# Kernel optimization log

Measured on AMD Instinct MI355X. Metric: run time of the kernel, lower is better.

## Reference

```python
import jax, jax.numpy as jnp
import numpy as np

V, H, NH, I, L, P = 32000, 1024, 16, 4096, 8, 2048
B, S = 2, 2048
DH = H // NH
EPS = 1e-5


def setup_inputs() -> dict:
    key = jax.random.key(0)
    ks = jax.random.split(key, 12)
    std = 0.02
    inp = {
        'input_ids': jax.random.randint(ks[0], (B, S), 0, V),
        'attention_mask': jnp.ones((B, S), dtype=jnp.float32),
        'tok_emb': jax.random.normal(ks[1], (V, H), jnp.float32) * std,
        'pos_emb': jax.random.normal(ks[2], (P, H), jnp.float32) * std,
        # per-layer params stacked on leading L dim (torch Linear convention: y = x @ W.T + b)
        'Wq': jax.random.normal(ks[3], (L, H, H), jnp.float32) * std,
        'bq': jnp.zeros((L, H), jnp.float32),
        'Wk': jax.random.normal(ks[4], (L, H, H), jnp.float32) * std,
        'bk': jnp.zeros((L, H), jnp.float32),
        'Wv': jax.random.normal(ks[5], (L, H, H), jnp.float32) * std,
        'bv': jnp.zeros((L, H), jnp.float32),
        'Wi': jax.random.normal(ks[6], (L, I, H), jnp.float32) * std,
        'bi': jnp.zeros((L, I), jnp.float32),
        'Wo': jax.random.normal(ks[7], (L, H, I), jnp.float32) * std,
        'bo': jnp.zeros((L, H), jnp.float32),
        'ln1_g': jnp.ones((L, H), jnp.float32),
        'ln1_b': jnp.zeros((L, H), jnp.float32),
        'ln2_g': jnp.ones((L, H), jnp.float32),
        'ln2_b': jnp.zeros((L, H), jnp.float32),
        'lnf_g': jnp.ones((H,), jnp.float32),
        'lnf_b': jnp.zeros((H,), jnp.float32),
        'Wlm': jax.random.normal(ks[8], (V, H), jnp.float32) * std,
    }
    return inp


def _layer_norm(x, g, b):
    m = jnp.mean(x, axis=-1, keepdims=True)
    v = jnp.var(x, axis=-1, keepdims=True)
    return (x - m) * jax.lax.rsqrt(v + EPS) * g + b


def reference(input_ids, attention_mask, tok_emb, pos_emb, Wq, bq, Wk, bk, Wv, bv,
              Wi, bi, Wo, bo, ln1_g, ln1_b, ln2_g, ln2_b, lnf_g, lnf_b, Wlm):
    b, s = input_ids.shape
    h = tok_emb[input_ids] + pos_emb[jnp.arange(s)][None, :, :]  # [B,S,H]
    mask = (1.0 - attention_mask)[:, None, None, :] * -10000.0   # [B,1,1,S]
    scale = 1.0 / (DH ** 0.5)

    def split_heads(x):  # [B,S,H] -> [B,NH,S,DH]
        return x.reshape(b, s, NH, DH).transpose(0, 2, 1, 3)

    def block(h, p):
        wq, bq_, wk, bk_, wv, bv_, wi, bi_, wo, bo_, g1, b1, g2, b2 = p
        q = split_heads(h @ wq.T + bq_)
        k = split_heads(h @ wk.T + bk_)
        v = split_heads(h @ wv.T + bv_)
        scores = jnp.einsum('bhqd,bhkd->bhqk', q, k) * scale + mask
        probs = jax.nn.softmax(scores, axis=-1)
        ctx = jnp.einsum('bhqk,bhkd->bhqd', probs, v)
        ctx = ctx.transpose(0, 2, 1, 3).reshape(b, s, H)
        h1 = _layer_norm(h + ctx, g1, b1)
        mlp = jax.nn.gelu(h1 @ wi.T + bi_, approximate=False) @ wo.T + bo_
        return _layer_norm(h1 + mlp, g2, b2), None

    h, _ = jax.lax.scan(block, h, (Wq, bq, Wk, bk, Wv, bv, Wi, bi, Wo, bo,
                                   ln1_g, ln1_b, ln2_g, ln2_b))
    h = _layer_norm(h, lnf_g, lnf_b)
    return h @ Wlm.T  # [B,S,V]
```

## Files before the change

kernel.cpp:

```cpp
#include <hip/hip_runtime.h>
#include <hip/hip_bf16.h>

#define V_ 32000
#define H_ 1024
#define NH_ 16
#define I_ 4096
#define L_ 8
#define B_ 2
#define S_ 2048
#define DH_ 64
#define M_ 4096
#define QS_ 3072

typedef __attribute__((ext_vector_type(4))) float f32x4;
typedef __attribute__((ext_vector_type(8))) short s16x8;

#define BARRIER() do { asm volatile("" ::: "memory"); __builtin_amdgcn_s_barrier(); asm volatile("" ::: "memory"); } while (0)
#define LGKM0()   do { asm volatile("s_waitcnt lgkmcnt(0)" ::: "memory"); __builtin_amdgcn_sched_barrier(0); } while (0)

__device__ __forceinline__ unsigned short f2b(float f) {
  union { float f; unsigned u; } x; x.f = f;
  return (unsigned short)((x.u + 0x7FFFu + ((x.u >> 16) & 1u)) >> 16);
}

__device__ __forceinline__ void gl_lds16(const unsigned short* g, unsigned short* l) {
  __builtin_amdgcn_global_load_lds(
      (__attribute__((address_space(1))) const void*)g,
      (__attribute__((address_space(3))) void*)l, 16, 0, 0);
}

__global__ __launch_bounds__(256) void wcvt(const float* __restrict__ src,
                                            unsigned short* __restrict__ dst) {
  size_t i = ((size_t)blockIdx.x * 256 + threadIdx.x) * 4;
  float4 v = *(const float4*)(src + i);
  ushort4 b;
  b.x = f2b(v.x); b.y = f2b(v.y); b.z = f2b(v.z); b.w = f2b(v.w);
  *(ushort4*)(dst + i) = b;
}

__global__ __launch_bounds__(256) void qkvcat_all(const float* __restrict__ q,
                                                  const float* __restrict__ k,
                                                  const float* __restrict__ v,
                                                  unsigned short* __restrict__ dst) {
  size_t i = ((size_t)blockIdx.x * 256 + threadIdx.x) * 4;
  size_t l = i / (3u * H_ * H_);
  size_t r = i - l * (3u * H_ * H_);
  const float* s; size_t off;
  if (r < (size_t)H_ * H_)          { s = q; off = l * H_ * H_ + r; }
  else if (r < 2u * H_ * H_)        { s = k; off = l * H_ * H_ + r - (size_t)H_ * H_; }
  else                              { s = v; off = l * H_ * H_ + r - 2u * H_ * H_; }
  float4 vv = *(const float4*)(s + off);
  ushort4 b;
  b.x = f2b(vv.x); b.y = f2b(vv.y); b.z = f2b(vv.z); b.w = f2b(vv.w);
  *(ushort4*)(dst + i) = b;
}

__global__ __launch_bounds__(256) void qkvcat(const float* __restrict__ q,
                                              const float* __restrict__ k,
                                              const float* __restrict__ v,
                                              unsigned short* __restrict__ dst) {
  int i = (blockIdx.x * 256 + threadIdx.x) * 4;
  const float* s; int off;
  if (i < H_ * H_)          { s = q; off = i; }
  else if (i < 2 * H_ * H_) { s = k; off = i - H_ * H_; }
  else                      { s = v; off = i - 2 * H_ * H_; }
  float4 vv = *(const float4*)(s + off);
  ushort4 b;
  b.x = f2b(vv.x); b.y = f2b(vv.y); b.z = f2b(vv.z); b.w = f2b(vv.w);
  *(ushort4*)(dst + i) = b;
}

__global__ __launch_bounds__(256) void bcat(const float* __restrict__ bq,
                                            const float* __restrict__ bk,
                                            const float* __restrict__ bv,
                                            float* __restrict__ dst) {
  int i = blockIdx.x * 256 + threadIdx.x;
  int l = i / (3 * H_), r = i - l * 3 * H_;
  int p = r >> 10, c = r & (H_ - 1);
  const float* s = (p == 0) ? bq : ((p == 1) ? bk : bv);
  dst[i] = s[l * H_ + c];
}

__global__ __launch_bounds__(256) void embed_kernel(
    const int* __restrict__ ids, const float* __restrict__ tok,
    const float* __restrict__ pos, float* __restrict__ h,
    unsigned short* __restrict__ xbf)
{
  int row = blockIdx.x;
  int c4 = threadIdx.x;
  int id = ids[row];
  int s = row & (S_ - 1);
  float4 tv = ((const float4*)(tok + (size_t)id * H_))[c4];
  float4 pv = ((const float4*)(pos + (size_t)s * H_))[c4];
  float4 v; v.x = tv.x + pv.x; v.y = tv.y + pv.y; v.z = tv.z + pv.z; v.w = tv.w + pv.w;
  ((float4*)(h + (size_t)row * H_))[c4] = v;
  ushort4 b; b.x = f2b(v.x); b.y = f2b(v.y); b.z = f2b(v.z); b.w = f2b(v.w);
  ((ushort4*)(xbf + (size_t)row * H_))[c4] = b;
}

template<int EPI>
__global__ __launch_bounds__(256) void gemm_bt(
    const unsigned short* __restrict__ A, const unsigned short* __restrict__ Wb,
    const float* __restrict__ bias, float* __restrict__ outf,
    unsigned short* __restrict__ outb, int M, int N, int K)
{
  __shared__ unsigned short As[128][32];
  __shared__ unsigned short Bs[128][32];
  int t = threadIdx.x;
  int lane = t & 63, wid = t >> 6;
  int m0 = blockIdx.x * 128, n0 = blockIdx.y * 128;
  int wm = (wid >> 1) * 64, wn = (wid & 1) * 64;
  int fr = lane & 15, kh = (lane >> 4) * 8;
  int lrow = lane >> 2, lcol = (lane & 3) * 8;

  f32x4 acc[4][4] = {};

  const unsigned short* Abase = A  + (size_t)(m0 + wid * 32 + lrow) * K + lcol;
  const unsigned short* Bbase = Wb + (size_t)(n0 + wid * 32 + lrow) * K + lcol;
  unsigned short* AL0 = &As[wid * 32][0];
  unsigned short* AL1 = &As[wid * 32 + 16][0];
  unsigned short* BL0 = &Bs[wid * 32][0];
  unsigned short* BL1 = &Bs[wid * 32 + 16][0];

  for (int k0 = 0; k0 < K; k0 += 32) {
    gl_lds16(Abase + k0,                     AL0);
    gl_lds16(Abase + k0 + (size_t)16 * K,    AL1);
    gl_lds16(Bbase + k0,                     BL0);
    gl_lds16(Bbase + k0 + (size_t)16 * K,    BL1);
    __syncthreads();
    s16x8 af[4], bfr[4];
    #pragma unroll
    for (int i = 0; i < 4; ++i) af[i]  = *(const s16x8*)(&As[wm + i * 16 + fr][kh]);
    #pragma unroll
    for (int j = 0; j < 4; ++j) bfr[j] = *(const s16x8*)(&Bs[wn + j * 16 + fr][kh]);
    #pragma unroll
    for (int i = 0; i < 4; ++i)
      #pragma unroll
      for (int j = 0; j < 4; ++j)
        acc[i][j] = __builtin_amdgcn_mfma_f32_16x16x32_bf16(af[i], bfr[j], acc[i][j], 0, 0, 0);
    __syncthreads();
  }

  int fq = lane >> 4;
  #pragma unroll
  for (int i = 0; i < 4; ++i) {
    #pragma unroll
    for (int j = 0; j < 4; ++j) {
      #pragma unroll
      for (int r = 0; r < 4; ++r) {
        int row = m0 + wm + i * 16 + fq * 4 + r;
        int col = n0 + wn + j * 16 + fr;
        float v = acc[i][j][r] + (bias ? bias[col] : 0.f);
        if (EPI == 0) {
          outf[(size_t)row * N + col] = v;
        } else if (EPI == 1) {
          float ge = 0.5f * v * (1.0f + erff(v * 0.70710678118f));
          outb[(size_t)row * N + col] = f2b(ge);
        } else {
          outb[(size_t)row * N + col] = f2b(v);
        }
      }
    }
  }
}

template<int EPI>
__global__ __launch_bounds__(512, 2) void gemm256(
    const unsigned short* __restrict__ A, const unsigned short* __restrict__ Wb,
    const float* __restrict__ bias, float* __restrict__ outf,
    unsigned short* __restrict__ outb, int M, int N, int K)
{
  __shared__ unsigned short ASm[2][16384];
  __shared__ unsigned short BSm[2][16384];

  const int t = threadIdx.x;
  const int lane = t & 63, wid = t >> 6;
  const int wm = wid >> 2, wn = wid & 3;
  const int fr = lane & 15, hi = lane >> 4;

  const int Nt = N >> 8;
  const int nwg = gridDim.x;
  const int cpx = nwg >> 3;
  int bid = (int)blockIdx.x;
  int swz = (bid & 7) * cpx + (bid >> 3);
  int band = swz / (4 * Nt);
  int rem = swz - band * (4 * Nt);
  const int m0 = (band * 4 + (rem & 3)) << 8;
  const int n0 = (rem >> 2) << 8;

  const int NT = K >> 6;

  const int srow = lane >> 3;
  const int scol = ((lane & 7) ^ srow) << 3;
  const int ch0 = wid * 2;

  const int axorb = (fr & 7) << 4;
  const int koe0 = ((hi * 16) ^ axorb) >> 1;
  const int koe1 = (((hi * 16) | 64) ^ axorb) >> 1;

  f32x4 acc[8][4] = {};

  auto stage_half = [&](int slot, int h, int k0) {
    if (h < 2) {
      const unsigned short* src =
          A + (size_t)(m0 + h * 128 + ch0 * 8 + srow) * K + k0 + scol;
      unsigned short* dst = &ASm[slot][(h * 128 + ch0 * 8) * 64];
      gl_lds16(src, dst);
      gl_lds16(src + (size_t)8 * K, dst + 8 * 64);
    } else {
      const unsigned short* src =
          Wb + (size_t)(n0 + (h - 2) * 128 + ch0 * 8 + srow) * K + k0 + scol;
      unsigned short* dst = &BSm[slot][((h - 2) * 128 + ch0 * 8) * 64];
      gl_lds16(src, dst);
      gl_lds16(src + (size_t)8 * K, dst + 8 * 64);
    }
  };

  stage_half(0, 0, 0); stage_half(0, 1, 0); stage_half(0, 2, 0); stage_half(0, 3, 0);
  if (NT > 1) { stage_half(1, 2, 64); stage_half(1, 3, 64); }

  s16x8 af[4][2], bfv[4][2];

  for (int T = 0; T < NT; ++T) {
    const int s = T & 1;
    const int k1 = (T + 1) << 6;

    if (T + 1 < NT) { asm volatile("s_waitcnt vmcnt(4)" ::: "memory"); }
    else            { asm volatile("s_waitcnt vmcnt(0)" ::: "memory"); }
    BARRIER();

    const unsigned short* As_ = ASm[s];
    const unsigned short* Bs_ = BSm[s];

    #pragma unroll
    for (int mi = 0; mi < 4; ++mi) {
      const unsigned short* p = As_ + (wm * 128 + mi * 16 + fr) * 64;
      af[mi][0] = *(const s16x8*)(p + koe0);
      af[mi][1] = *(const s16x8*)(p + koe1);
    }
    #pragma unroll
    for (int nj = 0; nj < 2; ++nj) {
      const unsigned short* p = Bs_ + (wn * 64 + nj * 16 + fr) * 64;
      bfv[nj][0] = *(const s16x8*)(p + koe0);
      bfv[nj][1] = *(const s16x8*)(p + koe1);
    }
    if (T + 1 < NT) stage_half(s ^ 1, 0, k1);
    BARRIER(); LGKM0();
    __builtin_amdgcn_s_setprio(1);
    #pragma unroll
    for (int mi = 0; mi < 4; ++mi)
      #pragma unroll
      for (int nj = 0; nj < 2; ++nj) {
        acc[mi][nj] = __builtin_amdgcn_mfma_f32_16x16x32_bf16(af[mi][0], bfv[nj][0], acc[mi][nj], 0, 0, 0);
        acc[mi][nj] = __builtin_amdgcn_mfma_f32_16x16x32_bf16(af[mi][1], bfv[nj][1], acc[mi][nj], 0, 0, 0);
      }
    __builtin_amdgcn_s_setprio(0);
    BARRIER();

    #pragma unroll
    for (int nj = 2; nj < 4; ++nj) {
      const unsigned short* p = Bs_ + (wn * 64 + nj * 16 + fr) * 64;
      bfv[nj][0] = *(const s16x8*)(p + koe0);
      bfv[nj][1] = *(const s16x8*)(p + koe1);
    }
    if (T + 1 < NT) stage_half(s ^ 1, 1, k1);
    BARRIER(); LGKM0();
    __builtin_amdgcn_s_setprio(1);
    #pragma unroll
    for (int mi = 0; mi < 4; ++mi)
      #pragma unroll
      for (int nj = 2; nj < 4; ++nj) {
        acc[mi][nj] = __builtin_amdgcn_mfma_f32_16x16x32_bf16(af[mi][0], bfv[nj][0], acc[mi][nj], 0, 0, 0);
        acc[mi][nj] = __builtin_amdgcn_mfma_f32_16x16x32_bf16(af[mi][1], bfv[nj][1], acc[mi][nj], 0, 0, 0);
      }
    __builtin_amdgcn_s_setprio(0);
    BARRIER();

    #pragma unroll
    for (int mi = 0; mi < 4; ++mi) {
      const unsigned short* p = As_ + (wm * 128 + (mi + 4) * 16 + fr) * 64;
      af[mi][0] = *(const s16x8*)(p + koe0);
      af[mi][1] = *(const s16x8*)(p + koe1);
    }
    if (T + 2 < NT) stage_half(s, 2, (T + 2) << 6);
    BARRIER(); LGKM0();
    __builtin_amdgcn_s_setprio(1);
    #pragma unroll
    for (int mi = 0; mi < 4; ++mi)
      #pragma unroll
      for (int nj = 2; nj < 4; ++nj) {
        acc[mi + 4][nj] = __builtin_amdgcn_mfma_f32_16x16x32_bf16(af[mi][0], bfv[nj][0], acc[mi + 4][nj], 0, 0, 0);
        acc[mi + 4][nj] = __builtin_amdgcn_mfma_f32_16x16x32_bf16(af[mi][1], bfv[nj][1], acc[mi + 4][nj], 0, 0, 0);
      }
    __builtin_amdgcn_s_setprio(0);
    BARRIER();

    if (T + 2 < NT) stage_half(s, 3, (T + 2) << 6);
    __builtin_amdgcn_s_setprio(1);
    #pragma unroll
    for (int mi = 0; mi < 4; ++mi)
      #pragma unroll
      for (int nj = 0; nj < 2; ++nj) {
        acc[mi + 4][nj] = __builtin_amdgcn_mfma_f32_16x16x32_bf16(af[mi][0], bfv[nj][0], acc[mi + 4][nj], 0, 0, 0);
        acc[mi + 4][nj] = __builtin_amdgcn_mfma_f32_16x16x32_bf16(af[mi][1], bfv[nj][1], acc[mi + 4][nj], 0, 0, 0);
      }
    __builtin_amdgcn_s_setprio(0);
  }

  #pragma unroll
  for (int mi = 0; mi < 8; ++mi) {
    #pragma unroll
    for (int nj = 0; nj < 4; ++nj) {
      #pragma unroll
      for (int r = 0; r < 4; ++r) {
        int row = m0 + wm * 128 + mi * 16 + hi * 4 + r;
        int col = n0 + wn * 64 + nj * 16 + fr;
        float v = acc[mi][nj][r] + (bias ? bias[col] : 0.f);
        if (EPI == 0) {
          outf[(size_t)row * N + col] = v;
        } else if (EPI == 1) {
          float ge = 0.5f * v * (1.0f + erff(v * 0.70710678118f));
          outb[(size_t)row * N + col] = f2b(ge);
        } else {
          outb[(size_t)row * N + col] = f2b(v);
        }
      }
    }
  }
}

__global__ __launch_bounds__(256) void transpose_v_bf16(
    const unsigned short* __restrict__ v, unsigned short* __restrict__ vT)
{
  __shared__ unsigned short tile[32][34];
  int bh = blockIdx.z;
  int b = bh >> 4, hh = bh & 15;
  const unsigned short* src = v + (size_t)b * S_ * QS_ + hh * DH_;
  unsigned short* dst = vT + (size_t)bh * DH_ * S_;
  int s0 = blockIdx.x * 32, d0 = blockIdx.y * 32;
  int x = threadIdx.x, y = threadIdx.y;
  #pragma unroll
  for (int i = 0; i < 4; ++i)
    tile[y + i * 8][x] = src[(size_t)(s0 + y + i * 8) * QS_ + d0 + x];
  __syncthreads();
  #pragma unroll
  for (int i = 0; i < 4; ++i)
    dst[(size_t)(d0 + y + i * 8) * S_ + s0 + x] = tile[x][y + i * 8];
}

#define KB_ 64
__global__ __launch_bounds__(512) void flash_mfma(
    const unsigned short* __restrict__ qb,
    const unsigned short* __restrict__ kb,
    const unsigned short* __restrict__ vtb,
    const float* __restrict__ mask,
    float* __restrict__ ctx)
{
  __shared__ unsigned short K2[2][KB_ * DH_];
  __shared__ unsigned short V2[2][DH_ * KB_];
  __shared__ unsigned short Ps[8][16][72];
  __shared__ float xpose[8][16];

  const float LOG2E = 1.4426950408889634f;
  const float SCL = 0.125f * LOG2E;
  int t = threadIdx.x, lane = t & 63, wid = t >> 6;
  int blk = blockIdx.x;
  int bh = blk & 31, qt = blk >> 5;
  int b = bh >> 4, hh = bh & 15;
  int row0 = b * S_ + qt * 128 + wid * 16;
  int fr = lane & 15, hi = lane >> 4;
  const float* mrow = mask + (size_t)b * S_;

  s16x8 qf[2];
  {
    const unsigned short* qrow = qb + (size_t)(row0 + fr) * QS_ + hh * DH_;
    qf[0] = *(const s16x8*)(qrow + hi * 8);
    qf[1] = *(const s16x8*)(qrow + 32 + hi * 8);
  }

  float m_run = -3.0e38f, l_run = 0.f;
  f32x4 octx[4] = {};

  const unsigned short* Kbase = kb + (size_t)b * S_ * QS_ + hh * DH_;
  const unsigned short* Vbase = vtb + (size_t)bh * DH_ * S_;

  int crow = lane >> 3;
  int scol = ((lane & 7) ^ crow) * 8;

  auto stage = [&](int slot, int t0) {
    gl_lds16(Kbase + (size_t)(t0 + wid * 8 + crow) * QS_ + scol, &K2[slot][wid * 512]);
    gl_lds16(Vbase + (size_t)(wid * 8 + crow) * S_ + t0 + scol,  &V2[slot][wid * 512]);
  };

  stage(0, 0);

  const int swz = (fr & 7) * 8;

  for (int t0 = 0; t0 < S_; t0 += KB_) {
    int slot = (t0 >> 6) & 1;
    __syncthreads();
    if (t0 + KB_ < S_) stage(slot ^ 1, t0 + KB_);

    f32x4 sacc[4] = {};
    #pragma unroll
    for (int g = 0; g < 4; ++g) {
      #pragma unroll
      for (int i = 0; i < 2; ++i) {
        s16x8 kf = *(const s16x8*)(&K2[slot][(g * 16 + fr) * 64 + ((i * 32 + hi * 8) ^ swz)]);
        sacc[g] = __builtin_amdgcn_mfma_f32_16x16x32_bf16(kf, qf[i], sacc[g], 0, 0, 0);
      }
    }

    float sc[4][4];
    float tm = -3.0e38f;
    #pragma unroll
    for (int g = 0; g < 4; ++g) {
      float4 mq = *(const float4*)(mrow + t0 + g * 16 + hi * 4);
      #pragma unroll
      for (int r = 0; r < 4; ++r) {
        float mk = (1.0f - ((const float*)&mq)[r]) * (-10000.0f * LOG2E);
        float v = sacc[g][r] * SCL + mk;
        sc[g][r] = v;
        tm = fmaxf(tm, v);
      }
    }
    tm = fmaxf(tm, __shfl_xor(tm, 16));
    tm = fmaxf(tm, __shfl_xor(tm, 32));

    if (!__all(tm <= m_run + 8.0f)) {
      float mn = fmaxf(m_run, tm);
      float corr = exp2f(m_run - mn);
      m_run = mn; l_run *= corr;
      xpose[wid][fr] = corr;
      float cr0 = xpose[wid][hi * 4 + 0];
      float cr1 = xpose[wid][hi * 4 + 1];
      float cr2 = xpose[wid][hi * 4 + 2];
      float cr3 = xpose[wid][hi * 4 + 3];
      #pragma unroll
      for (int dg = 0; dg < 4; ++dg) {
        octx[dg][0] *= cr0; octx[dg][1] *= cr1;
        octx[dg][2] *= cr2; octx[dg][3] *= cr3;
      }
    }

    float ps = 0.f;
    #pragma unroll
    for (int g = 0; g < 4; ++g)
      #pragma unroll
      for (int r = 0; r < 4; ++r) {
        float p = exp2f(sc[g][r] - m_run);
        sc[g][r] = p;
        ps += p;
      }
    ps += __shfl_xor(ps, 16);
    ps += __shfl_xor(ps, 32);
    l_run += ps;

    #pragma unroll
    for (int g = 0; g < 4; ++g) {
      uint2 pk;
      pk.x = (unsigned)f2b(sc[g][0]) | ((unsigned)f2b(sc[g][1]) << 16);
      pk.y = (unsigned)f2b(sc[g][2]) | ((unsigned)f2b(sc[g][3]) << 16);
      *(uint2*)(&Ps[wid][fr][g * 16 + hi * 4]) = pk;
    }

    #pragma unroll
    for (int kc = 0; kc < 2; ++kc) {
      s16x8 pf = *(const s16x8*)(&Ps[wid][fr][kc * 32 + hi * 8]);
      #pragma unroll
      for (int dg = 0; dg < 4; ++dg) {
        s16x8 vf2 = *(const s16x8*)(&V2[slot][(dg * 16 + fr) * 64 + ((kc * 32 + hi * 8) ^ swz)]);
        octx[dg] = __builtin_amdgcn_mfma_f32_16x16x32_bf16(pf, vf2, octx[dg], 0, 0, 0);
      }
    }
  }

  xpose[wid][fr] = l_run;
  float i0 = 1.0f / xpose[wid][hi * 4 + 0];
  float i1 = 1.0f / xpose[wid][hi * 4 + 1];
  float i2 = 1.0f / xpose[wid][hi * 4 + 2];
  float i3 = 1.0f / xpose[wid][hi * 4 + 3];
  #pragma unroll
  for (int dg = 0; dg < 4; ++dg) {
    size_t base = (size_t)(row0 + hi * 4) * H_ + hh * DH_ + dg * 16 + fr;
    ctx[base]          = octx[dg][0] * i0;
    ctx[base + H_]     = octx[dg][1] * i1;
    ctx[base + 2 * H_] = octx[dg][2] * i2;
    ctx[base + 3 * H_] = octx[dg][3] * i3;
  }
}

__global__ __launch_bounds__(256) void add_ln(
    const float* __restrict__ x, const float* __restrict__ y,
    const float* __restrict__ g, const float* __restrict__ bb,
    float* __restrict__ outf, unsigned short* __restrict__ outb)
{
  __shared__ float a1[4], a2[4];
  int row = blockIdx.x, t = threadIdx.x;
  float4 v = ((const float4*)(x + (size_t)row * H_))[t];
  if (y) {
    float4 u = ((const float4*)(y + (size_t)row * H_))[t];
    v.x += u.x; v.y += u.y; v.z += u.z; v.w += u.w;
  }
  float s1 = v.x + v.y + v.z + v.w;
  float s2 = v.x * v.x + v.y * v.y + v.z * v.z + v.w * v.w;
  #pragma unroll
  for (int d = 32; d; d >>= 1) { s1 += __shfl_xor(s1, d); s2 += __shfl_xor(s2, d); }
  if ((t & 63) == 0) { a1[t >> 6] = s1; a2[t >> 6] = s2; }
  __syncthreads();
  s1 = a1[0] + a1[1] + a1[2] + a1[3];
  s2 = a2[0] + a2[1] + a2[2] + a2[3];
  float mean = s1 * (1.0f / H_);
  float var = s2 * (1.0f / H_) - mean * mean;
  float inv = rsqrtf(var + 1e-5f);
  float4 gv = ((const float4*)g)[t];
  float4 bv = ((const float4*)bb)[t];
  float4 o;
  o.x = (v.x - mean) * inv * gv.x + bv.x;
  o.y = (v.y - mean) * inv * gv.y + bv.y;
  o.z = (v.z - mean) * inv * gv.z + bv.z;
  o.w = (v.w - mean) * inv * gv.w + bv.w;
  if (outf) ((float4*)(outf + (size_t)row * H_))[t] = o;
  if (outb) {
    ushort4 ob; ob.x = f2b(o.x); ob.y = f2b(o.y); ob.z = f2b(o.z); ob.w = f2b(o.w);
    ((ushort4*)(outb + (size_t)row * H_))[t] = ob;
  }
}

extern "C" void kernel_launch(void* const* d_in, const int* in_sizes, int n_in,
                              void* d_out, int out_size, void* d_ws, size_t ws_size,
                              hipStream_t stream) {
  const int*   ids  = (const int*)d_in[0];
  const float* mask = (const float*)d_in[1];
  const float* tok  = (const float*)d_in[2];
  const float* pos  = (const float*)d_in[3];
  const float* Wq   = (const float*)d_in[4];
  const float* bq   = (const float*)d_in[5];
  const float* Wk   = (const float*)d_in[6];
  const float* bk   = (const float*)d_in[7];
  const float* Wv   = (const float*)d_in[8];
  const float* bv   = (const float*)d_in[9];
  const float* Wi   = (const float*)d_in[10];
  const float* bi   = (const float*)d_in[11];
  const float* Wo   = (const float*)d_in[12];
  const float* bo   = (const float*)d_in[13];
  const float* ln1g = (const float*)d_in[14];
  const float* ln1b = (const float*)d_in[15];
  const float* ln2g = (const float*)d_in[16];
  const float* ln2b = (const float*)d_in[17];
  const float* lnfg = (const float*)d_in[18];
  const float* lnfb = (const float*)d_in[19];
  const float* Wlm  = (const float*)d_in[20];
  float* out = (float*)d_out;

  char* w = (char*)d_ws;
  size_t off = 0;
  auto alloc = [&](size_t bytes) { void* p = w + off; off = (off + bytes + 255) & ~(size_t)255; return p; };
  float* h     = (float*)alloc((size_t)M_ * H_ * 4);
  float* ctxb  = (float*)alloc((size_t)M_ * H_ * 4);
  unsigned short* qkvb  = (unsigned short*)alloc((size_t)M_ * QS_ * 2);
  unsigned short* vtb   = (unsigned short*)alloc((size_t)B_ * NH_ * DH_ * S_ * 2);
  unsigned short* xbf   = (unsigned short*)alloc((size_t)M_ * H_ * 2);
  unsigned short* midbf = (unsigned short*)alloc((size_t)M_ * I_ * 2);
  float* bqkv  = (float*)alloc((size_t)L_ * QS_ * 4);

  size_t wqkv_b = (size_t)L_ * 3 * H_ * H_ * 2;
  size_t wi_bb  = (size_t)L_ * I_ * H_ * 2;
  size_t wo_bb  = (size_t)L_ * H_ * I_ * 2;
  size_t wlm_bb = (size_t)V_ * H_ * 2;
  bool big = (ws_size - off) >= (wqkv_b + wi_bb + wo_bb + wlm_bb + 4 * 256);

  unsigned short *wqkv, *wi_a, *wo_a, *wlm_a, *wbuf = nullptr;
  if (big) {
    wqkv  = (unsigned short*)alloc(wqkv_b);
    wi_a  = (unsigned short*)alloc(wi_bb);
    wo_a  = (unsigned short*)alloc(wo_bb);
    wlm_a = (unsigned short*)alloc(wlm_bb);
    qkvcat_all<<<dim3((unsigned)((size_t)L_ * 3 * H_ * H_ / 1024)), 256, 0, stream>>>(Wq, Wk, Wv, wqkv);
    wcvt<<<dim3((unsigned)((size_t)L_ * I_ * H_ / 1024)), 256, 0, stream>>>(Wi, wi_a);
    wcvt<<<dim3((unsigned)((size_t)L_ * H_ * I_ / 1024)), 256, 0, stream>>>(Wo, wo_a);
    wcvt<<<dim3((unsigned)((size_t)V_ * H_ / 1024)), 256, 0, stream>>>(Wlm, wlm_a);
  } else {
    wbuf = (unsigned short*)alloc((size_t)V_ * H_ * 2);
  }

  bcat<<<dim3(L_ * QS_ / 256), 256, 0, stream>>>(bq, bk, bv, bqkv);
  embed_kernel<<<dim3(M_), 256, 0, stream>>>(ids, tok, pos, h, xbf);

  for (int l = 0; l < L_; ++l) {
    const unsigned short* wq_l;
    if (big) wq_l = wqkv + (size_t)l * 3 * H_ * H_;
    else {
      qkvcat<<<dim3(3 * H_ * H_ / 1024), 256, 0, stream>>>(
          Wq + (size_t)l * H_ * H_, Wk + (size_t)l * H_ * H_, Wv + (size_t)l * H_ * H_, wbuf);
      wq_l = wbuf;
    }
    gemm_bt<2><<<dim3(M_ / 128, QS_ / 128), 256, 0, stream>>>(
        xbf, wq_l, bqkv + (size_t)l * QS_, nullptr, qkvb, M_, QS_, H_);

    transpose_v_bf16<<<dim3(S_ / 32, DH_ / 32, B_ * NH_), dim3(32, 8), 0, stream>>>(
        qkvb + 2 * H_, vtb);
    flash_mfma<<<dim3(B_ * NH_ * S_ / 128), 512, 0, stream>>>(
        qkvb, qkvb + H_, vtb, mask, ctxb);

    add_ln<<<dim3(M_), 256, 0, stream>>>(h, ctxb, ln1g + l * H_, ln1b + l * H_, h, xbf);

    const unsigned short* wi_l;
    if (big) wi_l = wi_a + (size_t)l * I_ * H_;
    else {
      wcvt<<<dim3(I_ * H_ / 1024), 256, 0, stream>>>(Wi + (size_t)l * I_ * H_, wbuf);
      wi_l = wbuf;
    }
    gemm256<1><<<dim3((M_ / 256) * (I_ / 256)), 512, 0, stream>>>(
        xbf, wi_l, bi + l * I_, nullptr, midbf, M_, I_, H_);

    const unsigned short* wo_l;
    if (big) wo_l = wo_a + (size_t)l * H_ * I_;
    else {
      wcvt<<<dim3(H_ * I_ / 1024), 256, 0, stream>>>(Wo + (size_t)l * H_ * I_, wbuf);
      wo_l = wbuf;
    }
    gemm_bt<0><<<dim3(M_ / 128, H_ / 128), 256, 0, stream>>>(
        midbf, wo_l, bo + l * H_, ctxb, nullptr, M_, H_, I_);

    add_ln<<<dim3(M_), 256, 0, stream>>>(h, ctxb, ln2g + l * H_, ln2b + l * H_, h, xbf);
  }

  add_ln<<<dim3(M_), 256, 0, stream>>>(h, nullptr, lnfg, lnfb, nullptr, xbf);
  const unsigned short* wlm_l;
  if (big) wlm_l = wlm_a;
  else {
    wcvt<<<dim3(V_ * H_ / 1024), 256, 0, stream>>>(Wlm, wbuf);
    wlm_l = wbuf;
  }
  gemm256<0><<<dim3((M_ / 256) * (V_ / 256)), 512, 0, stream>>>(
      xbf, wlm_l, nullptr, out, nullptr, M_, V_, H_);
}
```

Measured before the change: 3.200 ms.

## Restructure GEMM main loop to single-stage prefetch with one barrier per K-step

Reworks the bf16 MFMA GEMM inner loop. Previously each K-step had four barrier-separated phases and prefetched half-tiles two steps ahead with a partial vmcnt wait. Now all B fragments and both halves of the A fragments are loaded into separate registers up front, and the next tile is staged into the other LDS buffer in four pieces between MFMA groups. There is one vmcnt(0) wait plus one barrier per step, and sched_barriers replace the inner barriers and lgkm waits. This cuts barrier and synchronisation overhead but shortens the prefetch distance, which may expose global-load latency, and raises register pressure.

```diff
diff --git a/kernel.cpp b/kernel.cpp
--- a/kernel.cpp
+++ b/kernel.cpp
@@ -16,7 +16,7 @@
 typedef __attribute__((ext_vector_type(8))) short s16x8;
 
 #define BARRIER() do { asm volatile("" ::: "memory"); __builtin_amdgcn_s_barrier(); asm volatile("" ::: "memory"); } while (0)
-#define LGKM0()   do { asm volatile("s_waitcnt lgkmcnt(0)" ::: "memory"); __builtin_amdgcn_sched_barrier(0); } while (0)
+#define SCHEDB()  __builtin_amdgcn_sched_barrier(0)
 
 __device__ __forceinline__ unsigned short f2b(float f) {
   union { float f; unsigned u; } x; x.f = f;
@@ -216,17 +216,16 @@
     }
   };
 
-  stage_half(0, 0, 0); stage_half(0, 1, 0); stage_half(0, 2, 0); stage_half(0, 3, 0);
-  if (NT > 1) { stage_half(1, 2, 64); stage_half(1, 3, 64); }
-
-  s16x8 af[4][2], bfv[4][2];
+  stage_half(0, 2, 0); stage_half(0, 3, 0); stage_half(0, 0, 0); stage_half(0, 1, 0);
+
+  s16x8 af0[4][2], af1[4][2], bfv[4][2];
 
   for (int T = 0; T < NT; ++T) {
     const int s = T & 1;
     const int k1 = (T + 1) << 6;
-
-    if (T + 1 < NT) { asm volatile("s_waitcnt vmcnt(4)" ::: "memory"); }
-    else            { asm volatile("s_waitcnt vmcnt(0)" ::: "memory"); }
+    const bool more = (T + 1 < NT);
+
+    asm volatile("s_waitcnt vmcnt(0)" ::: "memory");
     BARRIER();
 
     const unsigned short* As_ = ASm[s];
@@ -235,74 +234,69 @@
     #pragma unroll
     for (int mi = 0; mi < 4; ++mi) {
       const unsigned short* p = As_ + (wm * 128 + mi * 16 + fr) * 64;
-      af[mi][0] = *(const s16x8*)(p + koe0);
-      af[mi][1] = *(const s16x8*)(p + koe1);
-    }
-    #pragma unroll
-    for (int nj = 0; nj < 2; ++nj) {
+      af0[mi][0] = *(const s16x8*)(p + koe0);
+      af0[mi][1] = *(const s16x8*)(p + koe1);
+    }
+    #pragma unroll
+    for (int nj = 0; nj < 4; ++nj) {
       const unsigned short* p = Bs_ + (wn * 64 + nj * 16 + fr) * 64;
       bfv[nj][0] = *(const s16x8*)(p + koe0);
       bfv[nj][1] = *(const s16x8*)(p + koe1);
     }
-    if (T + 1 < NT) stage_half(s ^ 1, 0, k1);
-    BARRIER(); LGKM0();
+    if (more) stage_half(s ^ 1, 2, k1);
+    SCHEDB();
     __builtin_amdgcn_s_setprio(1);
     #pragma unroll
     for (int mi = 0; mi < 4; ++mi)
       #pragma unroll
       for (int nj = 0; nj < 2; ++nj) {
-        acc[mi][nj] = __builtin_amdgcn_mfma_f32_16x16x32_bf16(af[mi][0], bfv[nj][0], acc[mi][nj], 0, 0, 0);
-        acc[mi][nj] = __builtin_amdgcn_mfma_f32_16x16x32_bf16(af[mi][1], bfv[nj][1], acc[mi][nj], 0, 0, 0);
+        acc[mi][nj] = __builtin_amdgcn_mfma_f32_16x16x32_bf16(af0[mi][0], bfv[nj][0], acc[mi][nj], 0, 0, 0);
+        acc[mi][nj] = __builtin_amdgcn_mfma_f32_16x16x32_bf16(af0[mi][1], bfv[nj][1], acc[mi][nj], 0, 0, 0);
       }
     __builtin_amdgcn_s_setprio(0);
-    BARRIER();
-
-    #pragma unroll
-    for (int nj = 2; nj < 4; ++nj) {
-      const unsigned short* p = Bs_ + (wn * 64 + nj * 16 + fr) * 64;
-      bfv[nj][0] = *(const s16x8*)(p + koe0);
-      bfv[nj][1] = *(const s16x8*)(p + koe1);
-    }
-    if (T + 1 < NT) stage_half(s ^ 1, 1, k1);
-    BARRIER(); LGKM0();
-    __builtin_amdgcn_s_setprio(1);
-    #pragma unroll
-    for (int mi = 0; mi < 4; ++mi)
-      #pragma unroll
-      for (int nj = 2; nj < 4; ++nj) {
-        acc[mi][nj] = __builtin_amdgcn_mfma_f32_16x16x32_bf16(af[mi][0], bfv[nj][0], acc[mi][nj], 0, 0, 0);
-        acc[mi][nj] = __builtin_amdgcn_mfma_f32_16x16x32_bf16(af[mi][1], bfv[nj][1], acc[mi][nj], 0, 0, 0);
-      }
-    __builtin_amdgcn_s_setprio(0);
-    BARRIER();
+    SCHEDB();
 
     #pragma unroll
     for (int mi = 0; mi < 4; ++mi) {
       const unsigned short* p = As_ + (wm * 128 + (mi + 4) * 16 + fr) * 64;
-      af[mi][0] = *(const s16x8*)(p + koe0);
-      af[mi][1] = *(const s16x8*)(p + koe1);
-    }
-    if (T + 2 < NT) stage_half(s, 2, (T + 2) << 6);
-    BARRIER(); LGKM0();
+      af1[mi][0] = *(const s16x8*)(p + koe0);
+      af1[mi][1] = *(const s16x8*)(p + koe1);
+    }
+    if (more) stage_half(s ^ 1, 3, k1);
+    SCHEDB();
     __builtin_amdgcn_s_setprio(1);
     #pragma unroll
     for (int mi = 0; mi < 4; ++mi)
       #pragma unroll
       for (int nj = 2; nj < 4; ++nj) {
-        acc[mi + 4][nj] = __builtin_amdgcn_mfma_f32_16x16x32_bf16(af[mi][0], bfv[nj][0], acc[mi + 4][nj], 0, 0, 0);
-        acc[mi + 4][nj] = __builtin_amdgcn_mfma_f32_16x16x32_bf16(af[mi][1], bfv[nj][1], acc[mi + 4][nj], 0, 0, 0);
+        acc[mi][nj] = __builtin_amdgcn_mfma_f32_16x16x32_bf16(af0[mi][0], bfv[nj][0], acc[mi][nj], 0, 0, 0);
+        acc[mi][nj] = __builtin_amdgcn_mfma_f32_16x16x32_bf16(af0[mi][1], bfv[nj][1], acc[mi][nj], 0, 0, 0);
       }
     __builtin_amdgcn_s_setprio(0);
-    BARRIER();
-
-    if (T + 2 < NT) stage_half(s, 3, (T + 2) << 6);
+    SCHEDB();
+
+    if (more) stage_half(s ^ 1, 0, k1);
+    SCHEDB();
     __builtin_amdgcn_s_setprio(1);
     #pragma unroll
     for (int mi = 0; mi < 4; ++mi)
       #pragma unroll
+      for (int nj = 2; nj < 4; ++nj) {
+        acc[mi + 4][nj] = __builtin_amdgcn_mfma_f32_16x16x32_bf16(af1[mi][0], bfv[nj][0], acc[mi + 4][nj], 0, 0, 0);
+        acc[mi + 4][nj] = __builtin_amdgcn_mfma_f32_16x16x32_bf16(af1[mi][1], bfv[nj][1], acc[mi + 4][nj], 0, 0, 0);
+      }
+    __builtin_amdgcn_s_setprio(0);
+    SCHEDB();
+
+    if (more) stage_half(s ^ 1, 1, k1);
+    SCHEDB();
+    __builtin_amdgcn_s_setprio(1);
+    #pragma unroll
+    for (int mi = 0; mi < 4; ++mi)
+      #pragma unroll
       for (int nj = 0; nj < 2; ++nj) {
-        acc[mi + 4][nj] = __builtin_amdgcn_mfma_f32_16x16x32_bf16(af[mi][0], bfv[nj][0], acc[mi + 4][nj], 0, 0, 0);
-        acc[mi + 4][nj] = __builtin_amdgcn_mfma_f32_16x16x32_bf16(af[mi][1], bfv[nj][1], acc[mi + 4][nj], 0, 0, 0);
+        acc[mi + 4][nj] = __builtin_amdgcn_mfma_f32_16x16x32_bf16(af1[mi][0], bfv[nj][0], acc[mi + 4][nj], 0, 0, 0);
+        acc[mi + 4][nj] = __builtin_amdgcn_mfma_f32_16x16x32_bf16(af1[mi][1], bfv[nj][1], acc[mi + 4][nj], 0, 0, 0);
       }
     __builtin_amdgcn_s_setprio(0);
   }
```

Measured after the change: 3.255 ms. Within noise of the previous version (+1.7%).
